# Kernel optimization log

Measured on AMD Instinct MI355X. Metric: run time of the kernel, lower is better.

## Reference

```python
import jax, jax.numpy as jnp
import numpy as np

B, C, D, H, W = 1, 192, 32, 32, 32
NUM_HEADS = 6
KSZ = 3
DILATIONS = (1, 2, 3)
ND = len(DILATIONS)
HPD = NUM_HEADS // ND          # heads per dilation
HEAD_DIM = C // NUM_HEADS      # 32
CPD = C // ND                  # channels per dilation = HPD * HEAD_DIM
SCALE = HEAD_DIM ** -0.5
HIDDEN = int(C * 4.0)


def setup_inputs() -> dict:
    key = jax.random.key(0)
    ks = jax.random.split(key, 12)
    s = 0.02
    return {
        "x": jax.random.normal(ks[0], (B, C, H, W, D), jnp.float32),
        "qkv_w": jax.random.normal(ks[1], (3 * C, C), jnp.float32) * s,
        "proj_w": jax.random.normal(ks[2], (C, C), jnp.float32) * s,
        "proj_b": jnp.zeros((C,), jnp.float32),
        "g1": jnp.ones((C,), jnp.float32),
        "be1": jnp.zeros((C,), jnp.float32),
        "g2": jnp.ones((C,), jnp.float32),
        "be2": jnp.zeros((C,), jnp.float32),
        "w1": jax.random.normal(ks[3], (C, HIDDEN), jnp.float32) * s,
        "b1": jnp.zeros((HIDDEN,), jnp.float32),
        "w2": jax.random.normal(ks[4], (HIDDEN, C), jnp.float32) * s,
        "b2": jnp.zeros((C,), jnp.float32),
    }


def _layernorm(x, g, b, eps=1e-5):
    mu = jnp.mean(x, -1, keepdims=True)
    var = jnp.mean(jnp.square(x - mu), -1, keepdims=True)
    return (x - mu) * jax.lax.rsqrt(var + eps) * g + b


def _unfold3d(x, k, r):
    # x: [B, c, D, H, W] -> [k^3, B, c, D, H, W] of dilated local neighborhoods
    p = r * (k - 1) // 2
    xp = jnp.pad(x, ((0, 0), (0, 0), (p, p), (p, p), (p, p)))
    d, h, w = x.shape[2:]
    sl = [xp[:, :, i:i + d, j:j + h, l:l + w]
          for i in range(0, k * r, r)
          for j in range(0, k * r, r)
          for l in range(0, k * r, r)]
    return jnp.stack(sl, 0)


def _attn(x, qkv_w, proj_w, proj_b):
    # x: [B, D, H, W, C]
    x_cf = jnp.transpose(x, (0, 4, 1, 2, 3))                   # [B,C,D,H,W]
    qkv = jnp.einsum('oc,bczyx->bozyx', qkv_w, x_cf)
    qkv = qkv.reshape(B, 3, ND, CPD, D, H, W)
    outs = []
    for i, r in enumerate(DILATIONS):
        q = qkv[:, 0, i].reshape(B, HPD, HEAD_DIM, D, H, W)
        ku = _unfold3d(qkv[:, 1, i], KSZ, r).reshape(KSZ ** 3, B, HPD, HEAD_DIM, D, H, W)
        vu = _unfold3d(qkv[:, 2, i], KSZ, r).reshape(KSZ ** 3, B, HPD, HEAD_DIM, D, H, W)
        a = jnp.einsum('bnezyx,kbnezyx->bnzyxk', q, ku) * SCALE  # [B,n,D,H,W,27]
        a = jax.nn.softmax(a, axis=-1)
        o = jnp.einsum('bnzyxk,kbnezyx->bzyxne', a, vu).reshape(B, D, H, W, CPD)
        outs.append(o)
    out = jnp.concatenate(outs, -1)                            # [B,D,H,W,C] dilation-major
    return out @ proj_w + proj_b


def reference(x, qkv_w, proj_w, proj_b, g1, be1, g2, be2, w1, b1, w2, b2):
    # x: [B, C, H, W, D] -> [B, D, H, W, C]
    h = jnp.transpose(x, (0, 4, 2, 3, 1))
    h = h + _attn(_layernorm(h, g1, be1), qkv_w, proj_w, proj_b)
    m = _layernorm(h, g2, be2)
    m = jax.nn.gelu(m @ w1 + b1, approximate=False) @ w2 + b2
    h = h + m
    return jnp.transpose(h, (0, 4, 2, 3, 1))
```

## Files before the change

kernel.cpp:

```cpp
#include <hip/hip_runtime.h>
#include <hip/hip_bf16.h>
#include <math.h>

#define NV     32768
#define HIDDEN 768
#define SCALE  0.17677669529663687f

typedef __attribute__((ext_vector_type(8))) short short8;
typedef __attribute__((ext_vector_type(4))) float floatx4;
typedef __attribute__((ext_vector_type(8))) _Float16 h8;
typedef __attribute__((ext_vector_type(2))) _Float16 h2;
typedef __hip_bfloat16 bf16;

__device__ __forceinline__ void gload16(const void* g, void* l) {
    __builtin_amdgcn_global_load_lds(
        (const __attribute__((address_space(1))) unsigned int*)g,
        (__attribute__((address_space(3))) unsigned int*)l, 16, 0, 0);
}

__device__ __forceinline__ short f2bfs(float f) {
    bf16 b = __float2bfloat16(f);
    return *reinterpret_cast<short*>(&b);
}

__global__ __launch_bounds__(256) void prep_kernel(
        const float* __restrict__ qkv_w, const float* __restrict__ proj_w,
        const float* __restrict__ w1, const float* __restrict__ w2,
        bf16* __restrict__ wqkv, bf16* __restrict__ wproj,
        bf16* __restrict__ w1t, bf16* __restrict__ w2t) {
    int i = blockIdx.x * 256 + threadIdx.x;
    if (i < 110592) {
        wqkv[i] = (bf16)qkv_w[i];
    } else if (i < 147456) {
        int j = i - 110592; int r = j / 192, c = j - r * 192;
        wproj[c * 192 + r] = (bf16)proj_w[j];
    } else if (i < 294912) {
        int j = i - 147456; int r = j / 768, c = j - r * 768;
        w1t[c * 192 + r] = (bf16)w1[j];
    } else if (i < 442368) {
        int j = i - 294912; int r = j / 192, c = j - r * 192;
        w2t[c * 768 + r] = (bf16)w2[j];
    }
}

__global__ __launch_bounds__(256) void tin_ln_kernel(
        const float* __restrict__ xin, const float* __restrict__ g,
        const float* __restrict__ be, bf16* __restrict__ h,
        bf16* __restrict__ lnb) {
    __shared__ float lds[32 * 193];
    int yx = blockIdx.x;
    int y = yx >> 5, x = yx & 31;
    for (int idx = threadIdx.x; idx < 192 * 32; idx += 256) {
        int c = idx >> 5, z = idx & 31;
        lds[z * 193 + c] = xin[(((size_t)c * 32 + y) * 32 + x) * 32 + z];
    }
    __syncthreads();
    int wave = threadIdx.x >> 6, lane = threadIdx.x & 63;
    float ga = g[lane], gb = g[lane + 64], gc = g[lane + 128];
    float ba = be[lane], bb = be[lane + 64], bc = be[lane + 128];
    for (int z = wave; z < 32; z += 4) {
        float x0 = lds[z * 193 + lane];
        float x1 = lds[z * 193 + lane + 64];
        float x2 = lds[z * 193 + lane + 128];
        float s = x0 + x1 + x2;
        #pragma unroll
        for (int m = 32; m; m >>= 1) s += __shfl_xor(s, m);
        float mu = s * (1.f / 192.f);
        float d0 = x0 - mu, d1 = x1 - mu, d2 = x2 - mu;
        float s2 = d0 * d0 + d1 * d1 + d2 * d2;
        #pragma unroll
        for (int m = 32; m; m >>= 1) s2 += __shfl_xor(s2, m);
        float rstd = rsqrtf(s2 * (1.f / 192.f) + 1e-5f);
        size_t v = (size_t)((z << 10) + (y << 5) + x) * 192;
        h[v + lane]         = (bf16)x0;
        h[v + lane + 64]    = (bf16)x1;
        h[v + lane + 128]   = (bf16)x2;
        lnb[v + lane]       = (bf16)(d0 * rstd * ga + ba);
        lnb[v + lane + 64]  = (bf16)(d1 * rstd * gb + bb);
        lnb[v + lane + 128] = (bf16)(d2 * rstd * gc + bc);
    }
}

__global__ __launch_bounds__(256) void tout_kernel(const bf16* __restrict__ h,
                                                   float* __restrict__ outp) {
    __shared__ float lds[32 * 193];
    int yx = blockIdx.x;
    int y = yx >> 5, x = yx & 31;
    for (int idx = threadIdx.x; idx < 32 * 192; idx += 256) {
        int z = idx / 192, c = idx - z * 192;
        lds[z * 193 + c] = __bfloat162float(h[((size_t)((z * 32 + y) * 32 + x)) * 192 + c]);
    }
    __syncthreads();
    for (int idx = threadIdx.x; idx < 192 * 32; idx += 256) {
        int c = idx >> 5, z = idx & 31;
        outp[(((size_t)c * 32 + y) * 32 + x) * 32 + z] = lds[z * 193 + c];
    }
}

template <int MODE>
__global__ __launch_bounds__(256, 2) void mgemm_kernel(
        const bf16* __restrict__ A,
        const bf16* __restrict__ Bw,
        void* __restrict__ Cp,
        const float* __restrict__ bias,
        const bf16* __restrict__ res,
        int M, int N, int K) {
    __shared__ short Asm[128 * 64];
    __shared__ short Bsm[64 * 64];
    const int tid = threadIdx.x;
    const int lane = tid & 63;
    const int wave = tid >> 6;
    const int wm = wave >> 1, wn = wave & 1;
    const int m0 = blockIdx.x * 128;
    const int n0 = blockIdx.y * 64;

    const int srow = lane >> 3;
    const int scol = ((lane & 7) ^ ((lane >> 3) & 7)) * 16;

    floatx4 acc[4][2] = {};

    for (int k0 = 0; k0 < K; k0 += 64) {
        #pragma unroll
        for (int s = 0; s < 4; ++s) {
            int seg = wave * 4 + s;
            const char* g = (const char*)(A + (size_t)(m0 + seg * 8 + srow) * K + k0) + scol;
            gload16(g, (char*)Asm + seg * 1024);
        }
        #pragma unroll
        for (int s = 0; s < 2; ++s) {
            int seg = wave * 2 + s;
            const char* g = (const char*)(Bw + (size_t)(n0 + seg * 8 + srow) * K + k0) + scol;
            gload16(g, (char*)Bsm + seg * 1024);
        }
        __syncthreads();
        #pragma unroll
        for (int ks = 0; ks < 2; ++ks) {
            short8 af[4], bfr[2];
            const int cb = ks * 64 + (lane >> 4) * 16;
            #pragma unroll
            for (int i = 0; i < 4; ++i) {
                int row = wm * 64 + i * 16 + (lane & 15);
                af[i] = *reinterpret_cast<const short8*>(
                    (const char*)Asm + row * 128 + (cb ^ ((row & 7) << 4)));
            }
            #pragma unroll
            for (int j = 0; j < 2; ++j) {
                int row = wn * 32 + j * 16 + (lane & 15);
                bfr[j] = *reinterpret_cast<const short8*>(
                    (const char*)Bsm + row * 128 + (cb ^ ((row & 7) << 4)));
            }
            #pragma unroll
            for (int i = 0; i < 4; ++i)
                #pragma unroll
                for (int j = 0; j < 2; ++j)
                    acc[i][j] = __builtin_amdgcn_mfma_f32_16x16x32_bf16(
                        af[i], bfr[j], acc[i][j], 0, 0, 0);
        }
        __syncthreads();
    }

    const int r4 = (lane >> 4) * 4;
    const int cc = lane & 15;
    #pragma unroll
    for (int i = 0; i < 4; ++i) {
        #pragma unroll
        for (int j = 0; j < 2; ++j) {
            int colg = n0 + wn * 32 + j * 16 + cc;
            float bv = (MODE == 1 || MODE == 2) ? bias[colg] : 0.f;
            #pragma unroll
            for (int rg = 0; rg < 4; ++rg) {
                int rowg = m0 + wm * 64 + i * 16 + r4 + rg;
                float v = acc[i][j][rg];
                if (MODE == 1 || MODE == 2) v += bv;
                if (MODE == 2) v = 0.5f * v * (1.f + erff(v * 0.70710678118654752f));
                if (MODE == 1) {
                    v += __bfloat162float(res[(size_t)rowg * N + colg]);
                    ((bf16*)Cp)[(size_t)rowg * N + colg] = (bf16)v;
                } else if (MODE == 2) {
                    ((bf16*)Cp)[(size_t)rowg * N + colg] = (bf16)v;
                } else {
                    int part = colg / 192;
                    int rem  = colg - part * 192;
                    int di   = rem >> 6, hc = rem & 63;
                    size_t addr = (size_t)part * (6 * (size_t)NV * 32)
                                + (size_t)((di << 1) + (hc >> 5)) * ((size_t)NV * 32)
                                + (size_t)rowg * 32 + (hc & 31);
                    ((_Float16*)Cp)[addr] = (_Float16)v;
                }
            }
        }
    }
}

__global__ __launch_bounds__(256) void projln_kernel(
        const bf16* __restrict__ A, const bf16* __restrict__ Bw,
        bf16* __restrict__ hres, bf16* __restrict__ lnout,
        const float* __restrict__ bias,
        const float* __restrict__ g2, const float* __restrict__ be2) {
    __shared__ short Asm[64 * 64];
    __shared__ short Bsm[192 * 64];
    const int tid = threadIdx.x;
    const int lane = tid & 63;
    const int wave = tid >> 6;
    const int m0 = blockIdx.x * 64;

    const int srow = lane >> 3;
    const int scol = ((lane & 7) ^ ((lane >> 3) & 7)) * 16;

    floatx4 acc[12] = {};

    for (int k0 = 0; k0 < 192; k0 += 64) {
        #pragma unroll
        for (int s = 0; s < 2; ++s) {
            int seg = wave * 2 + s;
            const char* g = (const char*)(A + (size_t)(m0 + seg * 8 + srow) * 192 + k0) + scol;
            gload16(g, (char*)Asm + seg * 1024);
        }
        #pragma unroll
        for (int s = 0; s < 6; ++s) {
            int seg = wave * 6 + s;
            const char* g = (const char*)(Bw + (size_t)(seg * 8 + srow) * 192 + k0) + scol;
            gload16(g, (char*)Bsm + seg * 1024);
        }
        __syncthreads();
        #pragma unroll
        for (int ks = 0; ks < 2; ++ks) {
            const int cb = ks * 64 + (lane >> 4) * 16;
            int arow = wave * 16 + (lane & 15);
            short8 af = *reinterpret_cast<const short8*>(
                (const char*)Asm + arow * 128 + (cb ^ ((arow & 7) << 4)));
            #pragma unroll
            for (int j = 0; j < 12; ++j) {
                int brow = j * 16 + (lane & 15);
                short8 bfr = *reinterpret_cast<const short8*>(
                    (const char*)Bsm + brow * 128 + (cb ^ ((brow & 7) << 4)));
                acc[j] = __builtin_amdgcn_mfma_f32_16x16x32_bf16(af, bfr, acc[j], 0, 0, 0);
            }
        }
        __syncthreads();
    }

    const int cc = lane & 15;
    #pragma unroll
    for (int rg = 0; rg < 4; ++rg) {
        int rowg = m0 + wave * 16 + (lane >> 4) * 4 + rg;
        float vals[12];
        float vsum = 0.f;
        #pragma unroll
        for (int j = 0; j < 12; ++j) {
            int col = j * 16 + cc;
            float v = acc[j][rg] + bias[col]
                    + __bfloat162float(hres[(size_t)rowg * 192 + col]);
            vals[j] = v;
            vsum += v;
        }
        #pragma unroll
        for (int m = 8; m; m >>= 1) vsum += __shfl_xor(vsum, m);
        float mu = vsum * (1.f / 192.f);
        float vsq = 0.f;
        #pragma unroll
        for (int j = 0; j < 12; ++j) {
            float d = vals[j] - mu;
            vsq += d * d;
        }
        #pragma unroll
        for (int m = 8; m; m >>= 1) vsq += __shfl_xor(vsq, m);
        float rstd = rsqrtf(vsq * (1.f / 192.f) + 1e-5f);
        #pragma unroll
        for (int j = 0; j < 12; ++j) {
            int col = j * 16 + cc;
            hres[(size_t)rowg * 192 + col] = (bf16)vals[j];
            lnout[(size_t)rowg * 192 + col] =
                (bf16)((vals[j] - mu) * rstd * g2[col] + be2[col]);
        }
    }
}

__global__ __launch_bounds__(128) void attn_kernel(
        const _Float16* __restrict__ qa,
        const _Float16* __restrict__ ka,
        const _Float16* __restrict__ va,
        bf16* __restrict__ attn_out) {
    __shared__ _Float16 lds[9216];
    const int lin = blockIdx.x;
    const int swz = (lin & 7) * 768 + (lin >> 3);
    const int dh  = swz >> 10;
    const int yz  = swz & 1023;
    const int di = dh >> 1;
    const int r  = di + 1;
    const int z = yz >> 5, y = yz & 31;
    const int t = threadIdx.x;

    const _Float16* kb = ka + (size_t)dh * NV * 32;
    const _Float16* vb = va + (size_t)dh * NV * 32;

    #pragma unroll
    for (int s = 0; s < 9; ++s) {
        const int dz = s / 3 - 1, dy = s % 3 - 1;
        int zz = z + dz * r, yy = y + dy * r;
        zz = zz < 0 ? 0 : (zz > 31 ? 31 : zz);
        yy = yy < 0 ? 0 : (yy > 31 ? 31 : yy);
        const _Float16* src = kb + (size_t)(((zz << 10) + (yy << 5)) * 32);
        gload16((const char*)src + t * 16,
                (char*)lds + s * 2048 + (t >> 6) * 1024);
    }

    const int x = t >> 2, c4 = t & 3;
    const int v = (z << 10) + (y << 5) + x;
    h8 q8 = *reinterpret_cast<const h8*>(qa + ((size_t)dh * NV + v) * 32 + c4 * 8);
    h2 q01 = {q8[0], q8[1]}, q23 = {q8[2], q8[3]};
    h2 q45 = {q8[4], q8[5]}, q67 = {q8[6], q8[7]};

    __syncthreads();

    float denom = 0.f;
    h2 o01 = {0, 0}, o23 = {0, 0}, o45 = {0, 0}, o67 = {0, 0};
    const float cexp = SCALE * 1.44269504088896f;

    #pragma unroll
    for (int kk = 0; kk < 27; ++kk) {
        const int dz = kk / 9 - 1, dy = (kk / 3) % 3 - 1, dx = kk % 3 - 1;
        const int slot = (dz + 1) * 3 + (dy + 1);
        int nz = z + dz * r, ny = y + dy * r, nx = x + dx * r;
        bool ok = ((unsigned)nz < 32u) & ((unsigned)ny < 32u) & ((unsigned)nx < 32u);
        int rx = ok ? nx : x;
        int nvv = ok ? v + r * ((dz << 10) + (dy << 5) + dx) : v;
        h8 k8 = *reinterpret_cast<const h8*>(
            (const char*)lds + slot * 2048 + rx * 64 + c4 * 16);
        h8 v8 = *reinterpret_cast<const h8*>(vb + (size_t)nvv * 32 + c4 * 8);
        h2 a = q01 * (h2){k8[0], k8[1]};
        a = q23 * (h2){k8[2], k8[3]} + a;
        a = q45 * (h2){k8[4], k8[5]} + a;
        a = q67 * (h2){k8[6], k8[7]} + a;
        float d = (float)a[0] + (float)a[1];
        d += __shfl_xor(d, 1);
        d += __shfl_xor(d, 2);
        float p = exp2f(ok ? d * cexp : 0.f);
        denom += p;
        float w = ok ? p : 0.f;
        _Float16 wh = (_Float16)w;
        h2 w2 = {wh, wh};
        o01 = w2 * (h2){v8[0], v8[1]} + o01;
        o23 = w2 * (h2){v8[2], v8[3]} + o23;
        o45 = w2 * (h2){v8[4], v8[5]} + o45;
        o67 = w2 * (h2){v8[6], v8[7]} + o67;
    }
    float inv = 1.f / denom;

    bf16* op = attn_out + (size_t)v * 192 + di * 64 + (dh & 1) * 32 + c4 * 8;
    short8 st;
    st[0] = f2bfs((float)o01[0] * inv); st[1] = f2bfs((float)o01[1] * inv);
    st[2] = f2bfs((float)o23[0] * inv); st[3] = f2bfs((float)o23[1] * inv);
    st[4] = f2bfs((float)o45[0] * inv); st[5] = f2bfs((float)o45[1] * inv);
    st[6] = f2bfs((float)o67[0] * inv); st[7] = f2bfs((float)o67[1] * inv);
    *reinterpret_cast<short8*>(op) = st;
}

extern "C" void kernel_launch(void* const* d_in, const int* in_sizes, int n_in,
                              void* d_out, int out_size, void* d_ws, size_t ws_size,
                              hipStream_t stream) {
    const float* x      = (const float*)d_in[0];
    const float* qkv_w  = (const float*)d_in[1];
    const float* proj_w = (const float*)d_in[2];
    const float* proj_b = (const float*)d_in[3];
    const float* g1     = (const float*)d_in[4];
    const float* be1    = (const float*)d_in[5];
    const float* g2     = (const float*)d_in[6];
    const float* be2    = (const float*)d_in[7];
    const float* w1     = (const float*)d_in[8];
    const float* b1     = (const float*)d_in[9];
    const float* w2     = (const float*)d_in[10];
    const float* b2     = (const float*)d_in[11];
    float* out = (float*)d_out;

    char* p = (char*)d_ws;
    bf16* h     = (bf16*)p;  p += (size_t)NV * 192 * 2;
    bf16* lnb   = (bf16*)p;  p += (size_t)NV * 192 * 2;
    bf16* qkvb  = (bf16*)p;  p += (size_t)NV * 576 * 2;
    bf16* attnb = (bf16*)p;  p += (size_t)NV * 192 * 2;
    bf16* tb    = qkvb;
    bf16* wqkv  = (bf16*)p;  p += (size_t)576 * 192 * 2;
    bf16* wproj = (bf16*)p;  p += (size_t)192 * 192 * 2;
    bf16* w1t   = (bf16*)p;  p += (size_t)768 * 192 * 2;
    bf16* w2t   = (bf16*)p;  p += (size_t)192 * 768 * 2;

    _Float16* qa = (_Float16*)qkvb;
    _Float16* ka = qa + (size_t)6 * NV * 32;
    _Float16* va = qa + (size_t)12 * NV * 32;

    prep_kernel<<<(442368 + 255) / 256, 256, 0, stream>>>(
        qkv_w, proj_w, w1, w2, wqkv, wproj, w1t, w2t);
    tin_ln_kernel<<<1024, 256, 0, stream>>>(x, g1, be1, h, lnb);

    mgemm_kernel<3><<<dim3(NV / 128, 576 / 64), 256, 0, stream>>>(
        lnb, wqkv, qkvb, nullptr, nullptr, NV, 576, 192);
    attn_kernel<<<6144, 128, 0, stream>>>(qa, ka, va, attnb);
    projln_kernel<<<NV / 64, 256, 0, stream>>>(
        attnb, wproj, h, lnb, proj_b, g2, be2);

    mgemm_kernel<2><<<dim3(NV / 128, HIDDEN / 64), 256, 0, stream>>>(
        lnb, w1t, tb, b1, nullptr, NV, HIDDEN, 192);
    mgemm_kernel<1><<<dim3(NV / 128, 192 / 64), 256, 0, stream>>>(
        tb, w2t, h, b2, h, NV, 192, HIDDEN);

    tout_kernel<<<1024, 256, 0, stream>>>(h, out);
}
```

Before: 135.3 us.

## Replace LDS-staged GEMM with direct-to-register MFMA GEMM and compile-time K

The shared-memory tiled GEMM is replaced by a kernel where each wave loads its A and B fragments straight from global memory into registers and computes a 64x64 tile with 16 accumulators. K becomes a template parameter so the loop can be unrolled. This drops the LDS staging and the block barriers. In exchange, B tiles are no longer shared between waves through LDS, the 16-byte per-lane loads are strided rather than coalesced, and register pressure rises.

```diff
diff --git a/kernel.cpp b/kernel.cpp
--- a/kernel.cpp
+++ b/kernel.cpp
@@ -97,66 +97,41 @@
     }
 }
 
-template <int MODE>
-__global__ __launch_bounds__(256, 2) void mgemm_kernel(
+template <int MODE, int KK>
+__global__ __launch_bounds__(256) void dgemm_kernel(
         const bf16* __restrict__ A,
         const bf16* __restrict__ Bw,
         void* __restrict__ Cp,
         const float* __restrict__ bias,
         const bf16* __restrict__ res,
-        int M, int N, int K) {
-    __shared__ short Asm[128 * 64];
-    __shared__ short Bsm[64 * 64];
-    const int tid = threadIdx.x;
-    const int lane = tid & 63;
-    const int wave = tid >> 6;
-    const int wm = wave >> 1, wn = wave & 1;
-    const int m0 = blockIdx.x * 128;
+        int M, int N) {
+    const int lane = threadIdx.x & 63;
+    const int wave = threadIdx.x >> 6;
+    const int m0 = blockIdx.x * 256 + wave * 64;
     const int n0 = blockIdx.y * 64;
-
-    const int srow = lane >> 3;
-    const int scol = ((lane & 7) ^ ((lane >> 3) & 7)) * 16;
-
-    floatx4 acc[4][2] = {};
-
-    for (int k0 = 0; k0 < K; k0 += 64) {
-        #pragma unroll
-        for (int s = 0; s < 4; ++s) {
-            int seg = wave * 4 + s;
-            const char* g = (const char*)(A + (size_t)(m0 + seg * 8 + srow) * K + k0) + scol;
-            gload16(g, (char*)Asm + seg * 1024);
-        }
-        #pragma unroll
-        for (int s = 0; s < 2; ++s) {
-            int seg = wave * 2 + s;
-            const char* g = (const char*)(Bw + (size_t)(n0 + seg * 8 + srow) * K + k0) + scol;
-            gload16(g, (char*)Bsm + seg * 1024);
-        }
-        __syncthreads();
-        #pragma unroll
-        for (int ks = 0; ks < 2; ++ks) {
-            short8 af[4], bfr[2];
-            const int cb = ks * 64 + (lane >> 4) * 16;
+    const int rb = lane & 15;
+    const int kf = (lane >> 4) * 8;
+
+    const bf16* Ab = A + (size_t)(m0 + rb) * KK + kf;
+    const bf16* Bb = Bw + (size_t)(n0 + rb) * KK + kf;
+
+    floatx4 acc[4][4] = {};
+
+    #pragma unroll 6
+    for (int ks = 0; ks < KK / 32; ++ks) {
+        short8 af[4], bfr[4];
+        #pragma unroll
+        for (int i = 0; i < 4; ++i)
+            af[i] = *reinterpret_cast<const short8*>(Ab + (size_t)i * 16 * KK + ks * 32);
+        #pragma unroll
+        for (int j = 0; j < 4; ++j)
+            bfr[j] = *reinterpret_cast<const short8*>(Bb + (size_t)j * 16 * KK + ks * 32);
+        #pragma unroll
+        for (int i = 0; i < 4; ++i)
             #pragma unroll
-            for (int i = 0; i < 4; ++i) {
-                int row = wm * 64 + i * 16 + (lane & 15);
-                af[i] = *reinterpret_cast<const short8*>(
-                    (const char*)Asm + row * 128 + (cb ^ ((row & 7) << 4)));
-            }
-            #pragma unroll
-            for (int j = 0; j < 2; ++j) {
-                int row = wn * 32 + j * 16 + (lane & 15);
-                bfr[j] = *reinterpret_cast<const short8*>(
-                    (const char*)Bsm + row * 128 + (cb ^ ((row & 7) << 4)));
-            }
-            #pragma unroll
-            for (int i = 0; i < 4; ++i)
-                #pragma unroll
-                for (int j = 0; j < 2; ++j)
-                    acc[i][j] = __builtin_amdgcn_mfma_f32_16x16x32_bf16(
-                        af[i], bfr[j], acc[i][j], 0, 0, 0);
-        }
-        __syncthreads();
+            for (int j = 0; j < 4; ++j)
+                acc[i][j] = __builtin_amdgcn_mfma_f32_16x16x32_bf16(
+                    af[i], bfr[j], acc[i][j], 0, 0, 0);
     }
 
     const int r4 = (lane >> 4) * 4;
@@ -164,12 +139,12 @@
     #pragma unroll
     for (int i = 0; i < 4; ++i) {
         #pragma unroll
-        for (int j = 0; j < 2; ++j) {
-            int colg = n0 + wn * 32 + j * 16 + cc;
+        for (int j = 0; j < 4; ++j) {
+            int colg = n0 + j * 16 + cc;
             float bv = (MODE == 1 || MODE == 2) ? bias[colg] : 0.f;
             #pragma unroll
             for (int rg = 0; rg < 4; ++rg) {
-                int rowg = m0 + wm * 64 + i * 16 + r4 + rg;
+                int rowg = m0 + i * 16 + r4 + rg;
                 float v = acc[i][j][rg];
                 if (MODE == 1 || MODE == 2) v += bv;
                 if (MODE == 2) v = 0.5f * v * (1.f + erff(v * 0.70710678118654752f));
@@ -392,16 +367,16 @@
         qkv_w, proj_w, w1, w2, wqkv, wproj, w1t, w2t);
     tin_ln_kernel<<<1024, 256, 0, stream>>>(x, g1, be1, h, lnb);
 
-    mgemm_kernel<3><<<dim3(NV / 128, 576 / 64), 256, 0, stream>>>(
-        lnb, wqkv, qkvb, nullptr, nullptr, NV, 576, 192);
+    dgemm_kernel<3, 192><<<dim3(128, 9), 256, 0, stream>>>(
+        lnb, wqkv, qkvb, nullptr, nullptr, NV, 576);
     attn_kernel<<<6144, 128, 0, stream>>>(qa, ka, va, attnb);
     projln_kernel<<<NV / 64, 256, 0, stream>>>(
         attnb, wproj, h, lnb, proj_b, g2, be2);
 
-    mgemm_kernel<2><<<dim3(NV / 128, HIDDEN / 64), 256, 0, stream>>>(
-        lnb, w1t, tb, b1, nullptr, NV, HIDDEN, 192);
-    mgemm_kernel<1><<<dim3(NV / 128, 192 / 64), 256, 0, stream>>>(
-        tb, w2t, h, b2, h, NV, 192, HIDDEN);
+    dgemm_kernel<2, 192><<<dim3(128, 12), 256, 0, stream>>>(
+        lnb, w1t, tb, b1, nullptr, NV, HIDDEN);
+    dgemm_kernel<1, 768><<<dim3(128, 3), 256, 0, stream>>>(
+        tb, w2t, h, b2, h, NV, 192);
 
     tout_kernel<<<1024, 256, 0, stream>>>(h, out);
 }
```

Measured after the change: 202.7 us. 49.9% more time.
